# Performance work log

Hardware: AMD Instinct MI355X
Metric: run time of the kernel (lower is better)

The kernel has to match this reference:

```python
import jax, jax.numpy as jnp
import numpy as np
import math

B, NX, NY = 2, 2048, 2048
CX, CY = 1024, 1024
KEY_CH, VAL_CH, HEADS = 1024, 1024, 16


def setup_inputs() -> dict:
    key = jax.random.key(0)
    ks = jax.random.split(key, 10)
    s = lambda fan_in: 1.0 / math.sqrt(fan_in)
    inp = {
        "x": jax.random.normal(ks[0], (B, NX, CX), dtype=jnp.float32),
        "y": jax.random.normal(ks[1], (B, NY, CY), dtype=jnp.float32),
        "Wq": jax.random.uniform(ks[2], (CX, KEY_CH), jnp.float32, -s(CX), s(CX)),
        "bq": jax.random.uniform(ks[3], (KEY_CH,), jnp.float32, -s(CX), s(CX)),
        "Wk": jax.random.uniform(ks[4], (CY, KEY_CH), jnp.float32, -s(CY), s(CY)),
        "bk": jax.random.uniform(ks[5], (KEY_CH,), jnp.float32, -s(CY), s(CY)),
        "Wv": jax.random.uniform(ks[6], (CY, VAL_CH), jnp.float32, -s(CY), s(CY)),
        "bv": jax.random.uniform(ks[7], (VAL_CH,), jnp.float32, -s(CY), s(CY)),
        "Wo": jax.random.uniform(ks[8], (VAL_CH, CX), jnp.float32, -s(VAL_CH), s(VAL_CH)),
        "bo": jax.random.uniform(ks[9], (CX,), jnp.float32, -s(VAL_CH), s(VAL_CH)),
    }
    return inp


def reference(x, y, Wq, bq, Wk, bk, Wv, bv, Wo, bo):
    Bx, Nx, _ = x.shape
    By, Ny, _ = y.shape
    dk = KEY_CH // HEADS
    dv = VAL_CH // HEADS
    # projections
    q = (x @ Wq + bq).reshape(Bx, Nx, HEADS, dk)  # contiguous head slices == reshape
    k = (y @ Wk + bk).reshape(By, Ny, HEADS, dk)
    v = (y @ Wv + bv).reshape(By, Ny, HEADS, dv)
    # NOTE: original scales by 1/sqrt(Ny) (sequence length), not 1/sqrt(dk)
    scores = jnp.einsum("bnhd,bmhd->bhnm", q, k) / jnp.sqrt(jnp.float32(Ny))
    attn = jax.nn.softmax(scores, axis=-1)
    out = jnp.einsum("bhnm,bmhd->bnhd", attn, v).reshape(Bx, Nx, VAL_CH)
    out = jax.nn.relu(out @ Wo + bo)
    # dropout(p=0.2) is identity in eval mode
    return out
```

## Files before the change

kernel.cpp:

```cpp
#include <hip/hip_runtime.h>
#include <hip/hip_bf16.h>

typedef __bf16 bf16;
typedef __attribute__((ext_vector_type(8))) __bf16 bf16x8;
typedef __attribute__((ext_vector_type(4))) __bf16 bf16x4;
typedef __attribute__((ext_vector_type(4))) float f32x4;

__device__ __forceinline__ void gload_lds16(const void* g, void* l) {
  __builtin_amdgcn_global_load_lds((const __attribute__((address_space(1))) void*)g,
                                   (__attribute__((address_space(3))) void*)l, 16, 0, 0);
}

__global__ __launch_bounds__(256) void cvt2_kernel(const float4* __restrict__ a,
                                                   const float4* __restrict__ b,
                                                   bf16x4* __restrict__ oa,
                                                   bf16x4* __restrict__ ob, int n4) {
  int i = blockIdx.x * 256 + threadIdx.x;
  const float4* in = a; bf16x4* out = oa;
  if (i >= n4) { in = b; out = ob; i -= n4; }
  float4 v = in[i];
  bf16x4 o;
  o[0] = (bf16)v.x; o[1] = (bf16)v.y; o[2] = (bf16)v.z; o[3] = (bf16)v.w;
  out[i] = o;
}

__global__ __launch_bounds__(256) void wtrans_kernel(
    const float* __restrict__ W0, const float* __restrict__ W1,
    const float* __restrict__ W2, const float* __restrict__ W3,
    bf16* __restrict__ T0, bf16* __restrict__ T1,
    bf16* __restrict__ T2, bf16* __restrict__ T3) {
  const float* W; bf16* T;
  switch (blockIdx.z) {
    case 0: W = W0; T = T0; break;
    case 1: W = W1; T = T1; break;
    case 2: W = W2; T = T2; break;
    default: W = W3; T = T3; break;
  }
  __shared__ float t[32][33];
  int tx = threadIdx.x, ty = threadIdx.y;
  int bn = blockIdx.x * 32, bk = blockIdx.y * 32;
#pragma unroll
  for (int i = 0; i < 32; i += 8)
    t[ty + i][tx] = W[(size_t)(bk + ty + i) * 1024 + bn + tx];
  __syncthreads();
#pragma unroll
  for (int i = 0; i < 32; i += 8)
    T[(size_t)(bn + ty + i) * 1024 + bk + tx] = (bf16)t[tx][ty + i];
}

__global__ __launch_bounds__(256) void gemm_qkv(
    const bf16* __restrict__ xb, const bf16* __restrict__ yb,
    const bf16* __restrict__ Wqt, const bf16* __restrict__ Wkt, const bf16* __restrict__ Wvt,
    const float* __restrict__ bq, const float* __restrict__ bk, const float* __restrict__ bv,
    bf16* __restrict__ Qb, bf16* __restrict__ Kb, bf16* __restrict__ Vtb) {
  constexpr int K = 1024;
  __shared__ bf16 As[2][128 * 32];
  __shared__ bf16 Bs[2][128 * 32];
  const int z = blockIdx.z;
  const bf16* A  = (z == 0) ? xb : yb;
  const bf16* Bt = (z == 0) ? Wqt : (z == 1) ? Wkt : Wvt;
  const float* bias = (z == 0) ? bq : (z == 1) ? bk : bv;

  const int tid = threadIdx.x;
  const int wave = tid >> 6, lane = tid & 63;
  const int g = lane >> 4, r15 = lane & 15;
  const int m0 = blockIdx.x * 128, n0 = blockIdx.y * 128;
  const int wr = wave >> 1, wc = wave & 1;

  f32x4 acc[4][4] = {};

  const int c0 = tid, c1 = tid + 256;
  const int row0 = c0 >> 2, ch0 = c0 & 3;
  const int row1 = c1 >> 2, ch1 = c1 & 3;

  auto stage = [&](int buf, int k0) {
    gload_lds16(A  + (size_t)(m0 + row0) * K + k0 + ch0 * 8, (char*)As[buf] + c0 * 16);
    gload_lds16(Bt + (size_t)(n0 + row0) * K + k0 + ch0 * 8, (char*)Bs[buf] + c0 * 16);
    gload_lds16(A  + (size_t)(m0 + row1) * K + k0 + ch1 * 8, (char*)As[buf] + c1 * 16);
    gload_lds16(Bt + (size_t)(n0 + row1) * K + k0 + ch1 * 8, (char*)Bs[buf] + c1 * 16);
  };

  stage(0, 0);
  __syncthreads();
  int cur = 0;
  for (int t = 0; t < K / 32; ++t) {
    if (t + 1 < K / 32) stage(cur ^ 1, (t + 1) * 32);
    bf16x8 af[4], bfr[4];
#pragma unroll
    for (int mi = 0; mi < 4; ++mi)
      af[mi] = *(const bf16x8*)((const char*)As[cur] + ((wr * 64 + mi * 16 + r15) * 64 + g * 16));
#pragma unroll
    for (int nj = 0; nj < 4; ++nj)
      bfr[nj] = *(const bf16x8*)((const char*)Bs[cur] + ((wc * 64 + nj * 16 + r15) * 64 + g * 16));
#pragma unroll
    for (int mi = 0; mi < 4; ++mi)
#pragma unroll
      for (int nj = 0; nj < 4; ++nj)
        acc[mi][nj] = __builtin_amdgcn_mfma_f32_16x16x32_bf16(af[mi], bfr[nj], acc[mi][nj], 0, 0, 0);
    __syncthreads();
    cur ^= 1;
  }

#pragma unroll
  for (int mi = 0; mi < 4; ++mi) {
#pragma unroll
    for (int nj = 0; nj < 4; ++nj) {
      int row = m0 + wr * 64 + mi * 16 + g * 4;
      int col = n0 + wc * 64 + nj * 16 + r15;
      float bv_ = bias[col];
      if (z < 2) {
        bf16* C = (z == 0) ? Qb : Kb;
#pragma unroll
        for (int r = 0; r < 4; ++r)
          C[(size_t)(row + r) * 1024 + col] = (bf16)(acc[mi][nj][r] + bv_);
      } else {
        int b = row >> 11, n = row & 2047;
        bf16x4 pk;
#pragma unroll
        for (int r = 0; r < 4; ++r)
          pk[r] = (bf16)(acc[mi][nj][r] + bv_);
        *(bf16x4*)(Vtb + ((size_t)b * 1024 + col) * 2048 + n) = pk;
      }
    }
  }
}

__global__ __launch_bounds__(256) void gemm_out(
    const bf16* __restrict__ A, const bf16* __restrict__ Bt,
    const float* __restrict__ bias, float* __restrict__ C) {
  constexpr int K = 1024;
  __shared__ bf16 As[2][128 * 32];
  __shared__ bf16 Bs[2][64 * 32];
  const int tid = threadIdx.x;
  const int wave = tid >> 6, lane = tid & 63;
  const int g = lane >> 4, r15 = lane & 15;
  const int m0 = blockIdx.x * 128, n0 = blockIdx.y * 64;
  const int wr = wave >> 1, wc = wave & 1;

  f32x4 acc[4][2] = {};

  const int c0 = tid, c1 = tid + 256;
  const int row0 = c0 >> 2, ch0 = c0 & 3;
  const int row1 = c1 >> 2, ch1 = c1 & 3;

  auto stage = [&](int buf, int k0) {
    gload_lds16(A + (size_t)(m0 + row0) * K + k0 + ch0 * 8, (char*)As[buf] + c0 * 16);
    gload_lds16(A + (size_t)(m0 + row1) * K + k0 + ch1 * 8, (char*)As[buf] + c1 * 16);
    gload_lds16(Bt + (size_t)(n0 + row0) * K + k0 + ch0 * 8, (char*)Bs[buf] + c0 * 16);
  };

  stage(0, 0);
  __syncthreads();
  int cur = 0;
  for (int t = 0; t < K / 32; ++t) {
    if (t + 1 < K / 32) stage(cur ^ 1, (t + 1) * 32);
    bf16x8 af[4], bfr[2];
#pragma unroll
    for (int mi = 0; mi < 4; ++mi)
      af[mi] = *(const bf16x8*)((const char*)As[cur] + ((wr * 64 + mi * 16 + r15) * 64 + g * 16));
#pragma unroll
    for (int nj = 0; nj < 2; ++nj)
      bfr[nj] = *(const bf16x8*)((const char*)Bs[cur] + ((wc * 32 + nj * 16 + r15) * 64 + g * 16));
#pragma unroll
    for (int mi = 0; mi < 4; ++mi)
#pragma unroll
      for (int nj = 0; nj < 2; ++nj)
        acc[mi][nj] = __builtin_amdgcn_mfma_f32_16x16x32_bf16(af[mi], bfr[nj], acc[mi][nj], 0, 0, 0);
    __syncthreads();
    cur ^= 1;
  }

#pragma unroll
  for (int mi = 0; mi < 4; ++mi)
#pragma unroll
    for (int nj = 0; nj < 2; ++nj) {
      int row = m0 + wr * 64 + mi * 16 + g * 4;
      int col = n0 + wc * 32 + nj * 16 + r15;
      float bv_ = bias[col];
#pragma unroll
      for (int r = 0; r < 4; ++r)
        C[(size_t)(row + r) * 1024 + col] = fmaxf(acc[mi][nj][r] + bv_, 0.0f);
    }
}

__global__ __launch_bounds__(256, 4) void attn_kernel(
    const bf16* __restrict__ Q, const bf16* __restrict__ Kin,
    const bf16* __restrict__ Vt, bf16* __restrict__ Oa) {
  __shared__ bf16 Ks[2][64 * 64];
  __shared__ bf16 Vs[2][64 * 64];
  __shared__ char Ps[4][2048];
  const int tid = threadIdx.x;
  const int wave = tid >> 6, lane = tid & 63;
  const int g = lane >> 4, r15 = lane & 15;
  const int qt = blockIdx.x, bh = blockIdx.y;
  const int b = bh >> 4, h = bh & 15;
  const bf16* Qg = Q + ((size_t)b * 2048 + qt * 64) * 1024 + h * 64;
  const bf16* Kg = Kin + (size_t)b * 2048 * 1024 + h * 64;
  const bf16* Vg = Vt + ((size_t)b * 1024 + h * 64) * 2048;

  bf16x8 qf_[2];
#pragma unroll
  for (int kb = 0; kb < 2; ++kb)
    qf_[kb] = *(const bf16x8*)(Qg + (size_t)(wave * 16 + r15) * 1024 + kb * 32 + g * 8);

  f32x4 o[4] = {};
  float ls[4] = {};
  const float scale = 0.022097086912079612f;

  const int c0 = tid, c1 = tid + 256;
  const int srow0 = c0 >> 3, sch0 = (c0 & 7) ^ (srow0 & 7);
  const int srow1 = c1 >> 3, sch1 = (c1 & 7) ^ (srow1 & 7);

  auto stage = [&](int buf, int kv0) {
    gload_lds16(Kg + (size_t)(kv0 + srow0) * 1024 + sch0 * 8, (char*)Ks[buf] + c0 * 16);
    gload_lds16(Vg + (size_t)srow0 * 2048 + kv0 + sch0 * 8, (char*)Vs[buf] + c0 * 16);
    gload_lds16(Kg + (size_t)(kv0 + srow1) * 1024 + sch1 * 8, (char*)Ks[buf] + c1 * 16);
    gload_lds16(Vg + (size_t)srow1 * 2048 + kv0 + sch1 * 8, (char*)Vs[buf] + c1 * 16);
  };

  stage(0, 0);
  __syncthreads();
  int cur = 0;
  char* Pw = Ps[wave];

  for (int t = 0; t < 32; ++t) {
    if (t < 31) stage(cur ^ 1, (t + 1) * 64);

    f32x4 s[4] = {};
    __builtin_amdgcn_s_setprio(1);
#pragma unroll
    for (int kvf = 0; kvf < 4; ++kvf) {
      int row = kvf * 16 + r15;
#pragma unroll
      for (int kb = 0; kb < 2; ++kb) {
        int ch = (kb * 4 + g) ^ (row & 7);
        bf16x8 kf = *(const bf16x8*)((const char*)Ks[cur] + row * 128 + ch * 16);
        s[kvf] = __builtin_amdgcn_mfma_f32_16x16x32_bf16(qf_[kb], kf, s[kvf], 0, 0, 0);
      }
    }
    __builtin_amdgcn_s_setprio(0);

#pragma unroll
    for (int kvf = 0; kvf < 4; ++kvf)
#pragma unroll
      for (int r = 0; r < 4; ++r) {
        float p = __expf(s[kvf][r] * scale);
        ls[r] += p;
        int prow = g * 4 + r;
        int colb = (kvf * 16 + r15) * 2;
        *(bf16*)(Pw + prow * 128 + (colb ^ ((prow & 7) << 4))) = (bf16)p;
      }

    bf16x8 pa[2];
#pragma unroll
    for (int kb = 0; kb < 2; ++kb)
      pa[kb] = *(const bf16x8*)(Pw + r15 * 128 + ((kb * 64 + g * 16) ^ ((r15 & 7) << 4)));

    __builtin_amdgcn_s_setprio(1);
#pragma unroll
    for (int dvf = 0; dvf < 4; ++dvf) {
      int row = dvf * 16 + r15;
#pragma unroll
      for (int kb = 0; kb < 2; ++kb) {
        int ch = (kb * 4 + g) ^ (row & 7);
        bf16x8 vb = *(const bf16x8*)((const char*)Vs[cur] + row * 128 + ch * 16);
        o[dvf] = __builtin_amdgcn_mfma_f32_16x16x32_bf16(pa[kb], vb, o[dvf], 0, 0, 0);
      }
    }
    __builtin_amdgcn_s_setprio(0);

    __syncthreads();
    cur ^= 1;
  }

#pragma unroll
  for (int r = 0; r < 4; ++r) {
    float v = ls[r];
    v += __shfl_xor(v, 1);
    v += __shfl_xor(v, 2);
    v += __shfl_xor(v, 4);
    v += __shfl_xor(v, 8);
    ls[r] = v;
  }

#pragma unroll
  for (int dvf = 0; dvf < 4; ++dvf)
#pragma unroll
    for (int r = 0; r < 4; ++r) {
      float val = o[dvf][r] / ls[r];
      size_t row = (size_t)b * 2048 + qt * 64 + wave * 16 + g * 4 + r;
      Oa[row * 1024 + h * 64 + dvf * 16 + r15] = (bf16)val;
    }
}

extern "C" void kernel_launch(void* const* d_in, const int* in_sizes, int n_in,
                              void* d_out, int out_size, void* d_ws, size_t ws_size,
                              hipStream_t stream) {
  (void)in_sizes; (void)n_in; (void)out_size; (void)ws_size;
  const float* x  = (const float*)d_in[0];
  const float* y  = (const float*)d_in[1];
  const float* Wq = (const float*)d_in[2];
  const float* bq = (const float*)d_in[3];
  const float* Wk = (const float*)d_in[4];
  const float* bk = (const float*)d_in[5];
  const float* Wv = (const float*)d_in[6];
  const float* bv = (const float*)d_in[7];
  const float* Wo = (const float*)d_in[8];
  const float* bo = (const float*)d_in[9];

  char* ws = (char*)d_ws;
  bf16* xb  = (bf16*)(ws + 0);
  bf16* yb  = (bf16*)(ws + 8388608);
  bf16* Qb  = (bf16*)(ws + 16777216);
  bf16* Kb  = (bf16*)(ws + 25165824);
  bf16* Vtb = (bf16*)(ws + 33554432);
  bf16* Oab = (bf16*)(ws + 41943040);
  bf16* Wqt = (bf16*)(ws + 50331648);
  bf16* Wkt = (bf16*)(ws + 52428800);
  bf16* Wvt = (bf16*)(ws + 54525952);
  bf16* Wot = (bf16*)(ws + 56623104);

  const int n4 = 4096 * 1024 / 4;
  cvt2_kernel<<<2 * n4 / 256, 256, 0, stream>>>((const float4*)x, (const float4*)y,
                                                (bf16x4*)xb, (bf16x4*)yb, n4);
  wtrans_kernel<<<dim3(32, 32, 4), dim3(32, 8), 0, stream>>>(Wq, Wk, Wv, Wo, Wqt, Wkt, Wvt, Wot);
  gemm_qkv<<<dim3(32, 8, 3), 256, 0, stream>>>(xb, yb, Wqt, Wkt, Wvt, bq, bk, bv, Qb, Kb, Vtb);
  attn_kernel<<<dim3(32, 32), 256, 0, stream>>>(Qb, Kb, Vtb, Oab);
  gemm_out<<<dim3(32, 16), 256, 0, stream>>>(Oab, Wot, bo, (float*)d_out);
}
```

Baseline: 142.9 us.

## Rework attention with 32x32 MFMA, register-resident P, and folded exp2 scale

```diff
diff --git a/kernel.cpp b/kernel.cpp
--- a/kernel.cpp
+++ b/kernel.cpp
@@ -5,10 +5,24 @@
 typedef __attribute__((ext_vector_type(8))) __bf16 bf16x8;
 typedef __attribute__((ext_vector_type(4))) __bf16 bf16x4;
 typedef __attribute__((ext_vector_type(4))) float f32x4;
+typedef __attribute__((ext_vector_type(16))) float f32x16;
+typedef __attribute__((ext_vector_type(4))) unsigned int u32x4;
 
 __device__ __forceinline__ void gload_lds16(const void* g, void* l) {
   __builtin_amdgcn_global_load_lds((const __attribute__((address_space(1))) void*)g,
                                    (__attribute__((address_space(3))) void*)l, 16, 0, 0);
+}
+
+__device__ __forceinline__ float exp2_fast(float x) {
+  float r;
+  asm("v_exp_f32 %0, %1" : "=v"(r) : "v"(x));
+  return r;
+}
+
+__device__ __forceinline__ unsigned pk2(float a, float b) {
+  unsigned short lo = __builtin_bit_cast(unsigned short, (bf16)a);
+  unsigned short hi = __builtin_bit_cast(unsigned short, (bf16)b);
+  return (unsigned)lo | ((unsigned)hi << 16);
 }
 
 __global__ __launch_bounds__(256) void cvt2_kernel(const float4* __restrict__ a,
@@ -54,6 +68,7 @@
     const float* __restrict__ bq, const float* __restrict__ bk, const float* __restrict__ bv,
     bf16* __restrict__ Qb, bf16* __restrict__ Kb, bf16* __restrict__ Vtb) {
   constexpr int K = 1024;
+  constexpr float QSCALE = (float)(1.4426950408889634 / 45.254833995939045);
   __shared__ bf16 As[2][128 * 32];
   __shared__ bf16 Bs[2][128 * 32];
   const int z = blockIdx.z;
@@ -101,6 +116,7 @@
     cur ^= 1;
   }
 
+  const float scl = (z == 0) ? QSCALE : 1.0f;
 #pragma unroll
   for (int mi = 0; mi < 4; ++mi) {
 #pragma unroll
@@ -112,14 +128,14 @@
         bf16* C = (z == 0) ? Qb : Kb;
 #pragma unroll
         for (int r = 0; r < 4; ++r)
-          C[(size_t)(row + r) * 1024 + col] = (bf16)(acc[mi][nj][r] + bv_);
+          C[(size_t)(row + r) * 1024 + col] = (bf16)((acc[mi][nj][r] + bv_) * scl);
       } else {
         int b = row >> 11, n = row & 2047;
-        bf16x4 pk;
+        bf16x4 pkv;
 #pragma unroll
         for (int r = 0; r < 4; ++r)
-          pk[r] = (bf16)(acc[mi][nj][r] + bv_);
-        *(bf16x4*)(Vtb + ((size_t)b * 1024 + col) * 2048 + n) = pk;
+          pkv[r] = (bf16)(acc[mi][nj][r] + bv_);
+        *(bf16x4*)(Vtb + ((size_t)b * 1024 + col) * 2048 + n) = pkv;
       }
     }
   }
@@ -183,89 +199,92 @@
     }
 }
 
-__global__ __launch_bounds__(256, 4) void attn_kernel(
+__global__ __launch_bounds__(128, 2) void attn_kernel(
     const bf16* __restrict__ Q, const bf16* __restrict__ Kin,
     const bf16* __restrict__ Vt, bf16* __restrict__ Oa) {
   __shared__ bf16 Ks[2][64 * 64];
   __shared__ bf16 Vs[2][64 * 64];
-  __shared__ char Ps[4][2048];
   const int tid = threadIdx.x;
   const int wave = tid >> 6, lane = tid & 63;
-  const int g = lane >> 4, r15 = lane & 15;
-  const int qt = blockIdx.x, bh = blockIdx.y;
-  const int b = bh >> 4, h = bh & 15;
-  const bf16* Qg = Q + ((size_t)b * 2048 + qt * 64) * 1024 + h * 64;
-  const bf16* Kg = Kin + (size_t)b * 2048 * 1024 + h * 64;
-  const bf16* Vg = Vt + ((size_t)b * 1024 + h * 64) * 2048;
-
-  bf16x8 qf_[2];
-#pragma unroll
-  for (int kb = 0; kb < 2; ++kb)
-    qf_[kb] = *(const bf16x8*)(Qg + (size_t)(wave * 16 + r15) * 1024 + kb * 32 + g * 8);
-
-  f32x4 o[4] = {};
-  float ls[4] = {};
-  const float scale = 0.022097086912079612f;
-
-  const int c0 = tid, c1 = tid + 256;
-  const int srow0 = c0 >> 3, sch0 = (c0 & 7) ^ (srow0 & 7);
-  const int srow1 = c1 >> 3, sch1 = (c1 & 7) ^ (srow1 & 7);
+  const int q5 = lane & 31, h = lane >> 5;
+
+  int i = blockIdx.y * 32 + blockIdx.x;
+  int xcd = i & 7, slot = i >> 3;
+  int bh = xcd * 4 + (slot >> 5), qt = slot & 31;
+  int b = bh >> 4, hd = bh & 15;
+
+  const bf16* Qg = Q + ((size_t)b * 2048 + qt * 64 + wave * 32) * 1024 + hd * 64;
+  const bf16* Kg = Kin + (size_t)b * 2048 * 1024 + hd * 64;
+  const bf16* Vg = Vt + ((size_t)b * 1024 + hd * 64) * 2048;
+
+  bf16x8 qf[4];
+#pragma unroll
+  for (int ks = 0; ks < 4; ++ks)
+    qf[ks] = *(const bf16x8*)(Qg + (size_t)q5 * 1024 + ks * 16 + h * 8);
+
+  f32x16 o0 = {}, o1 = {};
+  float ls = 0.0f;
 
   auto stage = [&](int buf, int kv0) {
-    gload_lds16(Kg + (size_t)(kv0 + srow0) * 1024 + sch0 * 8, (char*)Ks[buf] + c0 * 16);
-    gload_lds16(Vg + (size_t)srow0 * 2048 + kv0 + sch0 * 8, (char*)Vs[buf] + c0 * 16);
-    gload_lds16(Kg + (size_t)(kv0 + srow1) * 1024 + sch1 * 8, (char*)Ks[buf] + c1 * 16);
-    gload_lds16(Vg + (size_t)srow1 * 2048 + kv0 + sch1 * 8, (char*)Vs[buf] + c1 * 16);
+#pragma unroll
+    for (int ii = 0; ii < 4; ++ii) {
+      int c = tid + ii * 128;
+      int row = c >> 3, ch = (c & 7) ^ (row & 7);
+      gload_lds16(Kg + (size_t)(kv0 + row) * 1024 + ch * 8, (char*)Ks[buf] + c * 16);
+      gload_lds16(Vg + (size_t)row * 2048 + kv0 + ch * 8, (char*)Vs[buf] + c * 16);
+    }
   };
 
   stage(0, 0);
   __syncthreads();
   int cur = 0;
-  char* Pw = Ps[wave];
 
   for (int t = 0; t < 32; ++t) {
     if (t < 31) stage(cur ^ 1, (t + 1) * 64);
 
-    f32x4 s[4] = {};
+    f32x16 s0 = {}, s1 = {};
     __builtin_amdgcn_s_setprio(1);
 #pragma unroll
-    for (int kvf = 0; kvf < 4; ++kvf) {
-      int row = kvf * 16 + r15;
-#pragma unroll
-      for (int kb = 0; kb < 2; ++kb) {
-        int ch = (kb * 4 + g) ^ (row & 7);
-        bf16x8 kf = *(const bf16x8*)((const char*)Ks[cur] + row * 128 + ch * 16);
-        s[kvf] = __builtin_amdgcn_mfma_f32_16x16x32_bf16(qf_[kb], kf, s[kvf], 0, 0, 0);
-      }
+    for (int ks = 0; ks < 4; ++ks) {
+      int chk = ((2 * ks + h) ^ (q5 & 7)) * 16;
+      bf16x8 k0 = *(const bf16x8*)((const char*)Ks[cur] + q5 * 128 + chk);
+      bf16x8 k1 = *(const bf16x8*)((const char*)Ks[cur] + (q5 + 32) * 128 + chk);
+      s0 = __builtin_amdgcn_mfma_f32_32x32x16_bf16(k0, qf[ks], s0, 0, 0, 0);
+      s1 = __builtin_amdgcn_mfma_f32_32x32x16_bf16(k1, qf[ks], s1, 0, 0, 0);
     }
     __builtin_amdgcn_s_setprio(0);
 
-#pragma unroll
-    for (int kvf = 0; kvf < 4; ++kvf)
-#pragma unroll
-      for (int r = 0; r < 4; ++r) {
-        float p = __expf(s[kvf][r] * scale);
-        ls[r] += p;
-        int prow = g * 4 + r;
-        int colb = (kvf * 16 + r15) * 2;
-        *(bf16*)(Pw + prow * 128 + (colb ^ ((prow & 7) << 4))) = (bf16)p;
-      }
-
-    bf16x8 pa[2];
-#pragma unroll
-    for (int kb = 0; kb < 2; ++kb)
-      pa[kb] = *(const bf16x8*)(Pw + r15 * 128 + ((kb * 64 + g * 16) ^ ((r15 & 7) << 4)));
+    unsigned pw0[4][2], pw1[4][2];
+#pragma unroll
+    for (int g4 = 0; g4 < 4; ++g4) {
+      float e0 = exp2_fast(s0[g4 * 4 + 0]), e1 = exp2_fast(s0[g4 * 4 + 1]);
+      float e2 = exp2_fast(s0[g4 * 4 + 2]), e3 = exp2_fast(s0[g4 * 4 + 3]);
+      float f0 = exp2_fast(s1[g4 * 4 + 0]), f1 = exp2_fast(s1[g4 * 4 + 1]);
+      float f2 = exp2_fast(s1[g4 * 4 + 2]), f3 = exp2_fast(s1[g4 * 4 + 3]);
+      ls += (e0 + e1) + (e2 + e3) + (f0 + f1) + (f2 + f3);
+      pw0[g4][0] = pk2(e0, e1); pw0[g4][1] = pk2(e2, e3);
+      pw1[g4][0] = pk2(f0, f1); pw1[g4][1] = pk2(f2, f3);
+    }
 
     __builtin_amdgcn_s_setprio(1);
 #pragma unroll
-    for (int dvf = 0; dvf < 4; ++dvf) {
-      int row = dvf * 16 + r15;
-#pragma unroll
-      for (int kb = 0; kb < 2; ++kb) {
-        int ch = (kb * 4 + g) ^ (row & 7);
-        bf16x8 vb = *(const bf16x8*)((const char*)Vs[cur] + row * 128 + ch * 16);
-        o[dvf] = __builtin_amdgcn_mfma_f32_16x16x32_bf16(pa[kb], vb, o[dvf], 0, 0, 0);
-      }
+    for (int ks = 0; ks < 4; ++ks) {
+      const unsigned (*pw)[2] = (ks < 2) ? pw0 : pw1;
+      const int base = (ks & 1) * 2;
+      unsigned a0 = pw[base][0], a1 = pw[base][1];
+      unsigned b0 = pw[base + 1][0], b1 = pw[base + 1][1];
+      unsigned s0w = h ? a0 : b0, s1w = h ? a1 : b1;
+      unsigned r0 = __shfl_xor(s0w, 32), r1 = __shfl_xor(s1w, 32);
+      unsigned o0w = h ? b0 : a0, o1w = h ? b1 : a1;
+      u32x4 w;
+      w[0] = h ? r0 : o0w; w[1] = h ? r1 : o1w;
+      w[2] = h ? o0w : r0; w[3] = h ? o1w : r1;
+      bf16x8 pa = __builtin_bit_cast(bf16x8, w);
+      int chk = ((2 * ks + h) ^ (q5 & 7)) * 16;
+      bf16x8 v0 = *(const bf16x8*)((const char*)Vs[cur] + q5 * 128 + chk);
+      bf16x8 v1 = *(const bf16x8*)((const char*)Vs[cur] + (q5 + 32) * 128 + chk);
+      o0 = __builtin_amdgcn_mfma_f32_32x32x16_bf16(pa, v0, o0, 0, 0, 0);
+      o1 = __builtin_amdgcn_mfma_f32_32x32x16_bf16(pa, v1, o1, 0, 0, 0);
     }
     __builtin_amdgcn_s_setprio(0);
 
@@ -273,23 +292,19 @@
     cur ^= 1;
   }
 
-#pragma unroll
-  for (int r = 0; r < 4; ++r) {
-    float v = ls[r];
-    v += __shfl_xor(v, 1);
-    v += __shfl_xor(v, 2);
-    v += __shfl_xor(v, 4);
-    v += __shfl_xor(v, 8);
-    ls[r] = v;
-  }
-
-#pragma unroll
-  for (int dvf = 0; dvf < 4; ++dvf)
+  ls += __shfl_xor(ls, 32);
+  float inv = __builtin_amdgcn_rcpf(ls);
+
+#pragma unroll
+  for (int g4 = 0; g4 < 4; ++g4)
 #pragma unroll
     for (int r = 0; r < 4; ++r) {
-      float val = o[dvf][r] / ls[r];
-      size_t row = (size_t)b * 2048 + qt * 64 + wave * 16 + g * 4 + r;
-      Oa[row * 1024 + h * 64 + dvf * 16 + r15] = (bf16)val;
+      int qr = g4 * 8 + 4 * h + r;
+      float il = __shfl(inv, qr);
+      size_t row = (size_t)b * 2048 + qt * 64 + wave * 32 + qr;
+      bf16* dst = Oa + row * 1024 + hd * 64;
+      dst[q5]      = (bf16)(o0[g4 * 4 + r] * il);
+      dst[q5 + 32] = (bf16)(o1[g4 * 4 + r] * il);
     }
 }
 
@@ -325,6 +340,6 @@
                                                 (bf16x4*)xb, (bf16x4*)yb, n4);
   wtrans_kernel<<<dim3(32, 32, 4), dim3(32, 8), 0, stream>>>(Wq, Wk, Wv, Wo, Wqt, Wkt, Wvt, Wot);
   gemm_qkv<<<dim3(32, 8, 3), 256, 0, stream>>>(xb, yb, Wqt, Wkt, Wvt, bq, bk, bv, Qb, Kb, Vtb);
-  attn_kernel<<<dim3(32, 32), 256, 0, stream>>>(Qb, Kb, Vtb, Oab);
+  attn_kernel<<<dim3(32, 32), dim3(128), 0, stream>>>(Qb, Kb, Vtb, Oab);
   gemm_out<<<dim3(32, 16), 256, 0, stream>>>(Oab, Wot, bo, (float*)d_out);
 }
```

Result: no change. 141.6 us (-0.9%).
